# Performance work log

Measured on AMD Instinct MI355X. Metric: run time of the kernel, lower is better.

Reference implementation:

```python
import jax, jax.numpy as jnp
import numpy as np

D_MODEL = 2048
N_HEADS = 16
D_HEAD = D_MODEL // N_HEADS
B, S = 4, 2048


def setup_inputs() -> dict:
    key = jax.random.key(0)
    ks = jax.random.split(key, 5)
    scale = 1.0 / np.sqrt(D_MODEL)
    return {
        "x": jax.random.normal(ks[0], (B, S, D_MODEL), dtype=jnp.float32),
        "w_qkv": jax.random.normal(ks[1], (D_MODEL, 3 * D_MODEL), dtype=jnp.float32) * scale,
        "b_qkv": jax.random.normal(ks[2], (3 * D_MODEL,), dtype=jnp.float32) * 0.01,
        "w_out": jax.random.normal(ks[3], (D_MODEL, D_MODEL), dtype=jnp.float32) * scale,
        "b_out": jax.random.normal(ks[4], (D_MODEL,), dtype=jnp.float32) * 0.01,
    }


def reference(x, w_qkv, b_qkv, w_out, b_out):
    b, s, d = x.shape
    qkv = x @ w_qkv + b_qkv                      # [b, s, 3d]
    q, k, v = jnp.split(qkv, 3, axis=-1)
    # [b, h, s, dh]
    q = q.reshape(b, s, N_HEADS, D_HEAD).transpose(0, 2, 1, 3)
    k = k.reshape(b, s, N_HEADS, D_HEAD).transpose(0, 2, 1, 3)
    v = v.reshape(b, s, N_HEADS, D_HEAD).transpose(0, 2, 1, 3)
    # past_kv is None -> s_past == s
    scale = 1.0 / np.sqrt(D_HEAD).astype(np.float32)
    scores = jnp.einsum("bhqd,bhkd->bhqk", q, k) * scale  # [b, h, s, s]
    # causal mask: disallow j > i (diagonal = 1 + s_past - s = 1)
    causal = jnp.tril(jnp.ones((s, s), dtype=bool))
    scores = jnp.where(causal, scores, jnp.float32(-jnp.inf))
    attn = jax.nn.softmax(scores, axis=-1)
    out = jnp.einsum("bhqk,bhkd->bhqd", attn, v)          # [b, h, s, dh]
    out = out.transpose(0, 2, 1, 3).reshape(b, s, d)
    out = out @ w_out + b_out
    return out, k, v
```

## Files before the change

### kernel.cpp

```cpp
#include <hip/hip_runtime.h>
#include <hip/hip_bf16.h>
#include <cstdint>

typedef unsigned short u16;
typedef unsigned int u32;
typedef __attribute__((ext_vector_type(4))) float f32x4;
typedef __attribute__((ext_vector_type(8))) __bf16 bf16x8;

#define DEVFN static __device__ __forceinline__

constexpr int Bb = 4, S = 2048, Dm = 2048, H = 16, DH = 128;
constexpr int M  = Bb * S;
constexpr int N3 = 3 * Dm;
constexpr int KK = 2048;
constexpr float ATTN_SCALE = 0.088388347648318447f;
constexpr float LOG2E = 1.4426950408889634f;

DEVFN u16 f2bf(float f) {
  union { float f; u32 u; } v; v.f = f;
  u32 u = v.u;
  return (u16)((u + 0x7fffu + ((u >> 16) & 1u)) >> 16);
}

DEVFN void async16(const void* g, void* l) {
  __builtin_amdgcn_global_load_lds(
      (__attribute__((address_space(1))) unsigned int*)(g),
      (__attribute__((address_space(3))) unsigned int*)(l), 16, 0, 0);
}


__global__ __launch_bounds__(256) void k_cvt_bf16(const float* __restrict__ in,
                                                  u16* __restrict__ out, int n) {
  int i = (blockIdx.x * 256 + threadIdx.x) * 4;
  if (i < n) {
    float4 f = *(const float4*)(in + i);
    ushort4 o;
    o.x = f2bf(f.x); o.y = f2bf(f.y); o.z = f2bf(f.z); o.w = f2bf(f.w);
    *(ushort4*)(out + i) = o;
  }
}

__global__ __launch_bounds__(256) void k_transpose_bf16(const float* __restrict__ in,
                                                        u16* __restrict__ out,
                                                        int R, int C) {
  __shared__ float tile[32][33];
  int c0 = blockIdx.x * 32, r0 = blockIdx.y * 32;
  int tx = threadIdx.x & 31, ty = threadIdx.x >> 5;
#pragma unroll
  for (int i = 0; i < 4; i++)
    tile[ty + 8 * i][tx] = in[(size_t)(r0 + ty + 8 * i) * C + c0 + tx];
  __syncthreads();
#pragma unroll
  for (int i = 0; i < 4; i++)
    out[(size_t)(c0 + ty + 8 * i) * R + r0 + tx] = f2bf(tile[tx][ty + 8 * i]);
}


#define RA(buf, half) ((buf) * 65536 + (half) * 16384)
#define RB(buf, half) ((buf) * 65536 + 32768 + (half) * 16384)

#define BARRIER() __builtin_amdgcn_s_barrier()
#define LGK0() { asm volatile("s_waitcnt lgkmcnt(0)" ::: "memory"); __builtin_amdgcn_sched_barrier(0); }
#define VMC2() { asm volatile("s_waitcnt vmcnt(2)" ::: "memory"); __builtin_amdgcn_sched_barrier(0); }
#define VMC0() { asm volatile("s_waitcnt vmcnt(0)" ::: "memory"); __builtin_amdgcn_sched_barrier(0); }

template <int BUF, int QUAD>
DEVFN void ldAq(const char* lds, int wm, int lrow, int lkg, bf16x8 af[4][2]) {
  const char* base = lds + RA(BUF, 0) + wm * 16384;
  const int sw = (lrow & 7) << 4;
#pragma unroll
  for (int mi = 0; mi < 4; mi++) {
    int row = QUAD * 64 + mi * 16 + lrow;
#pragma unroll
    for (int kk = 0; kk < 2; kk++)
      af[mi][kk] = *(const bf16x8*)(base + row * 128 + ((kk * 64 + lkg * 16) ^ sw));
  }
}

template <int BUF, int NS>
DEVFN void ldB(const char* lds, int wn, int lrow, int lkg, bf16x8 b[2][2]) {
  const char* base = lds + RB(BUF, 0) + (wn >> 1) * 16384;
  const int sw = (lrow & 7) << 4;
#pragma unroll
  for (int ni = 0; ni < 2; ni++) {
    int row = (wn & 1) * 64 + NS * 32 + ni * 16 + lrow;
#pragma unroll
    for (int kk = 0; kk < 2; kk++)
      b[ni][kk] = *(const bf16x8*)(base + row * 128 + ((kk * 64 + lkg * 16) ^ sw));
  }
}

template <int MS, int NS>
DEVFN void mmq(f32x4 acc[8][4], bf16x8 af[4][2], bf16x8 b[2][2]) {
  __builtin_amdgcn_s_setprio(1);
#pragma unroll
  for (int kk = 0; kk < 2; kk++)
#pragma unroll
    for (int mi = 0; mi < 4; mi++)
#pragma unroll
      for (int ni = 0; ni < 2; ni++)
        acc[MS * 4 + mi][NS * 2 + ni] = __builtin_amdgcn_mfma_f32_16x16x32_bf16(
            af[mi][kk], b[ni][kk], acc[MS * 4 + mi][NS * 2 + ni], 0, 0, 0);
  __builtin_amdgcn_s_setprio(0);
}

template <int MODE>
__global__ __launch_bounds__(512, 2) void k_gemm(
    const u16* __restrict__ A, const u16* __restrict__ BT,
    const float* __restrict__ bias, float* __restrict__ Cf,
    u16* __restrict__ q_bf, u16* __restrict__ k_bf, u16* __restrict__ v_bfT,
    int N) {
  __shared__ __align__(16) char lds[131072];
  char* ldsc = lds;
  const int tid = threadIdx.x;
  const int wid = tid >> 6, lane = tid & 63;
  const int wm = wid >> 2, wn = wid & 3;
  const int lrow = lane & 15, lkg = lane >> 4;

  const int bid = blockIdx.x;
  const int xcd = bid & 7;
  const int i = bid >> 3;
  const int r = i & 15;
  const int j = i >> 4;
  const int tm0 = (xcd * 4 + (r >> 2)) << 8;
  const int tn0 = (j * 4 + (r & 3)) << 8;

  const int NT = KK >> 6;

  const int srow = tid >> 3;
  const int scol = (((tid & 7) * 16) ^ ((srow & 7) << 4)) >> 1;
  const int dstoff = (tid & ~63) * 16;
  const u16* bA0 = A + (size_t)(tm0 + srow) * KK + scol;
  const u16* bA1 = A + (size_t)(tm0 + 128 + srow) * KK + scol;
  const u16* bB0 = BT + (size_t)(tn0 + srow) * KK + scol;
  const u16* bB1 = BT + (size_t)(tn0 + 128 + srow) * KK + scol;

  auto stage2 = [&](const u16* src, int region) {
    async16(src, ldsc + region + dstoff);
    async16(src + (size_t)64 * KK, ldsc + region + 8192 + dstoff);
  };

  f32x4 acc[8][4] = {};
  bf16x8 afA[4][2], afB[4][2], b0[2][2], b1[2][2];

  stage2(bA0, RA(0, 0));
  stage2(bA1, RA(0, 1));
  stage2(bB0, RB(0, 0));
  stage2(bB1, RB(0, 1));
  stage2(bA0 + 64, RA(1, 0));
  VMC2();
  BARRIER();

  for (int it = 0; it < NT / 2; it++) {
    const int t = 2 * it;
    const int t1 = (t + 1) * 64;
    const int t2 = (t + 2 < NT) ? (t + 2) * 64 : 0;
    const int t3 = (t + 3 < NT) ? (t + 3) * 64 : 0;

    ldAq<0, 0>(ldsc, wm, lrow, lkg, afA);
    ldB<0, 0>(ldsc, wn, lrow, lkg, b0);
    stage2(bA1 + t1, RA(1, 1));
    BARRIER(); LGK0();
    mmq<0, 0>(acc, afA, b0);
    BARRIER();

    ldB<0, 1>(ldsc, wn, lrow, lkg, b1);
    stage2(bB0 + t1, RB(1, 0));
    BARRIER(); LGK0();
    mmq<0, 1>(acc, afA, b1);
    BARRIER();

    ldAq<0, 1>(ldsc, wm, lrow, lkg, afB);
    stage2(bB1 + t1, RB(1, 1));
    BARRIER(); LGK0();
    mmq<1, 1>(acc, afB, b1);
    BARRIER();

    stage2(bA0 + t2, RA(0, 0));
    VMC2();
    BARRIER();
    mmq<1, 0>(acc, afB, b0);
    BARRIER();

    ldAq<1, 0>(ldsc, wm, lrow, lkg, afA);
    ldB<1, 0>(ldsc, wn, lrow, lkg, b0);
    stage2(bA1 + t2, RA(0, 1));
    BARRIER(); LGK0();
    mmq<0, 0>(acc, afA, b0);
    BARRIER();

    ldB<1, 1>(ldsc, wn, lrow, lkg, b1);
    stage2(bB0 + t2, RB(0, 0));
    BARRIER(); LGK0();
    mmq<0, 1>(acc, afA, b1);
    BARRIER();

    ldAq<1, 1>(ldsc, wm, lrow, lkg, afB);
    stage2(bB1 + t2, RB(0, 1));
    BARRIER(); LGK0();
    mmq<1, 1>(acc, afB, b1);
    BARRIER();

    stage2(bA0 + t3, RA(1, 0));
    VMC2();
    BARRIER();
    mmq<1, 0>(acc, afB, b0);
    BARRIER();
  }
  VMC0();

  if (MODE == 0) {
#pragma unroll
    for (int mig = 0; mig < 8; mig++) {
      int row = tm0 + wm * 128 + (mig >> 2) * 64 + (mig & 3) * 16 + lkg * 4;
#pragma unroll
      for (int nig = 0; nig < 4; nig++) {
        int col = tn0 + wn * 64 + (nig >> 1) * 32 + (nig & 1) * 16 + lrow;
        float bv = bias[col];
#pragma unroll
        for (int r2 = 0; r2 < 4; r2++)
          Cf[(size_t)(row + r2) * N + col] = acc[mig][nig][r2] + bv;
      }
    }
  } else {
#pragma unroll
    for (int mig = 0; mig < 8; mig++) {
      int row = tm0 + wm * 128 + (mig >> 2) * 64 + (mig & 3) * 16 + lkg * 4;
#pragma unroll
      for (int nig = 0; nig < 4; nig++) {
        int n = tn0 + wn * 64 + (nig >> 1) * 32 + (nig & 1) * 16 + lrow;
        float bv = bias[n];
        int type = n >> 11;
        int d = n & 2047;
        int h = d >> 7, dh = d & 127;
#pragma unroll
        for (int r2 = 0; r2 < 4; r2++) {
          int rr = row + r2;
          int b = rr >> 11, s = rr & 2047;
          float val = acc[mig][nig][r2] + bv;
          size_t idx = ((size_t)(b * H + h) * S + s) * DH + dh;
          if (type == 0) {
            q_bf[idx] = f2bf(val * ATTN_SCALE);
          } else if (type == 1) {
            Cf[(size_t)M * Dm + idx] = val;
            k_bf[idx] = f2bf(val);
          } else {
            Cf[(size_t)2 * M * Dm + idx] = val;
            v_bfT[((size_t)(b * H + h) * DH + dh) * S + s] = f2bf(val);
          }
        }
      }
    }
  }
}

__global__ __launch_bounds__(256, 2) void k_attn(const u16* __restrict__ q_bf,
                                                 const u16* __restrict__ k_bf,
                                                 const u16* __restrict__ v_bfT,
                                                 u16* __restrict__ attn_bf) {
  __shared__ u16 ldsK[2][64 * 128];
  __shared__ u16 ldsV[2][128 * 64];
  __shared__ u16 ldsP[4][32 * 64];

  const int tid = threadIdx.x;
  const int wid = tid >> 6, lane = tid & 63;
  const int lrow = lane & 15, lkg = lane >> 4;

  const int bid = blockIdx.x;
  const int xcd = bid & 7;
  const int ii = bid >> 3;
  const int bh = xcd * 8 + (ii >> 4);
  const int qi = 15 - (ii & 15);
  const int b = bh >> 4, h = bh & 15;
  const int wq0 = qi * 128 + wid * 32;
  const int swz = (lrow & 7) << 4;

  const u16* qp = q_bf + (size_t)bh * S * DH;
  const u16* kp = k_bf + (size_t)bh * S * DH;
  const u16* vp = v_bfT + (size_t)bh * DH * S;

  bf16x8 qf[2][4];
#pragma unroll
  for (int qt = 0; qt < 2; qt++)
#pragma unroll
    for (int kk = 0; kk < 4; kk++)
      qf[qt][kk] = *(const bf16x8*)(qp + (size_t)(wq0 + qt * 16 + lrow) * DH +
                                    kk * 32 + lkg * 8);

  float mr[2][4], lr[2][4];
#pragma unroll
  for (int qt = 0; qt < 2; qt++)
#pragma unroll
    for (int r = 0; r < 4; r++) { mr[qt][r] = -1e30f; lr[qt][r] = 0.f; }
  f32x4 oacc[2][8] = {};

  const int nkb = qi * 2 + 2;

  auto stage = [&](int kb, int buf) {
#pragma unroll
    for (int i = 0; i < 4; i++) {
      int L = i * 4096 + wid * 1024 + lane * 16;
      int krow = L >> 8, kch = (L >> 4) & 15;
      async16(kp + (size_t)(kb * 64 + krow) * DH + ((kch ^ (krow & 7)) * 8),
              (char*)ldsK[buf] + L);
      int vd = L >> 7, vch = (L >> 4) & 7;
      async16(vp + (size_t)vd * S + kb * 64 + ((vch ^ (vd & 7)) * 8),
              (char*)ldsV[buf] + L);
    }
  };

  stage(0, 0);
  asm volatile("s_waitcnt vmcnt(0)" ::: "memory");
  __builtin_amdgcn_s_barrier();

  int cur = 0;
  for (int kb = 0; kb < nkb; kb++) {
    if (kb + 1 < nkb) stage(kb + 1, cur ^ 1);

    if (kb * 64 <= wq0 + 31) {
      const u16* Kc = ldsK[cur];
      const u16* Vc = ldsV[cur];
      f32x4 sacc[2][4] = {};
      __builtin_amdgcn_s_setprio(1);
#pragma unroll
      for (int kt = 0; kt < 4; kt++)
#pragma unroll
        for (int kk = 0; kk < 4; kk++) {
          bf16x8 kf = *(const bf16x8*)((const char*)Kc +
                        (kt * 16 + lrow) * 256 + ((kk * 64 + lkg * 16) ^ swz));
          sacc[0][kt] = __builtin_amdgcn_mfma_f32_16x16x32_bf16(qf[0][kk], kf,
                                                                sacc[0][kt], 0, 0, 0);
          sacc[1][kt] = __builtin_amdgcn_mfma_f32_16x16x32_bf16(qf[1][kk], kf,
                                                                sacc[1][kt], 0, 0, 0);
        }
      __builtin_amdgcn_s_setprio(0);

      if (kb * 64 + 63 > wq0) {
#pragma unroll
        for (int qt = 0; qt < 2; qt++)
#pragma unroll
          for (int kt = 0; kt < 4; kt++) {
            int k = kb * 64 + kt * 16 + lrow;
#pragma unroll
            for (int r = 0; r < 4; r++)
              if (k > wq0 + qt * 16 + lkg * 4 + r) sacc[qt][kt][r] = -1e30f;
          }
      }

      float pm[2][4];
#pragma unroll
      for (int qt = 0; qt < 2; qt++)
#pragma unroll
        for (int r = 0; r < 4; r++)
          pm[qt][r] = fmaxf(fmaxf(sacc[qt][0][r], sacc[qt][1][r]),
                            fmaxf(sacc[qt][2][r], sacc[qt][3][r]));
#pragma unroll
      for (int off = 1; off < 16; off <<= 1)
#pragma unroll
        for (int qt = 0; qt < 2; qt++)
#pragma unroll
          for (int r = 0; r < 4; r++)
            pm[qt][r] = fmaxf(pm[qt][r], __shfl_xor(pm[qt][r], off, 64));

      float dmax = pm[0][0] - mr[0][0];
#pragma unroll
      for (int qt = 0; qt < 2; qt++)
#pragma unroll
        for (int r = 0; r < 4; r++)
          dmax = fmaxf(dmax, pm[qt][r] - mr[qt][r]);
      if (!__all(dmax <= 8.0f)) {
        float sc[2][4];
#pragma unroll
        for (int qt = 0; qt < 2; qt++)
#pragma unroll
          for (int r = 0; r < 4; r++) {
            float mn = fmaxf(mr[qt][r], pm[qt][r]);
            sc[qt][r] = exp2f((mr[qt][r] - mn) * LOG2E);
            mr[qt][r] = mn;
            lr[qt][r] *= sc[qt][r];
          }
#pragma unroll
        for (int qt = 0; qt < 2; qt++)
#pragma unroll
          for (int nd = 0; nd < 8; nd++)
#pragma unroll
            for (int r = 0; r < 4; r++) oacc[qt][nd][r] *= sc[qt][r];
      }

      float rs[2][4] = {};
#pragma unroll
      for (int qt = 0; qt < 2; qt++)
#pragma unroll
        for (int kt = 0; kt < 4; kt++)
#pragma unroll
          for (int r = 0; r < 4; r++) {
            float p = exp2f((sacc[qt][kt][r] - mr[qt][r]) * LOG2E);
            rs[qt][r] += p;
            int prow = qt * 16 + lkg * 4 + r;
            *(u16*)((char*)ldsP[wid] + prow * 128 +
                    (((kt * 16 + lrow) * 2) ^ ((prow & 7) << 4))) = f2bf(p);
          }
#pragma unroll
      for (int off = 1; off < 16; off <<= 1)
#pragma unroll
        for (int qt = 0; qt < 2; qt++)
#pragma unroll
          for (int r = 0; r < 4; r++)
            rs[qt][r] += __shfl_xor(rs[qt][r], off, 64);
#pragma unroll
      for (int qt = 0; qt < 2; qt++)
#pragma unroll
        for (int r = 0; r < 4; r++)
          lr[qt][r] += rs[qt][r];

      asm volatile("s_waitcnt lgkmcnt(0)" ::: "memory");
      bf16x8 pf[2][2];
#pragma unroll
      for (int qt = 0; qt < 2; qt++)
#pragma unroll
        for (int kk = 0; kk < 2; kk++)
          pf[qt][kk] = *(const bf16x8*)((const char*)ldsP[wid] +
                         (qt * 16 + lrow) * 128 + ((kk * 64 + lkg * 16) ^ swz));
      __builtin_amdgcn_s_setprio(1);
#pragma unroll
      for (int nd = 0; nd < 8; nd++) {
        bf16x8 vf0 = *(const bf16x8*)((const char*)Vc +
                       (nd * 16 + lrow) * 128 + ((lkg * 16) ^ swz));
        bf16x8 vf1 = *(const bf16x8*)((const char*)Vc +
                       (nd * 16 + lrow) * 128 + ((64 + lkg * 16) ^ swz));
#pragma unroll
        for (int qt = 0; qt < 2; qt++) {
          oacc[qt][nd] = __builtin_amdgcn_mfma_f32_16x16x32_bf16(pf[qt][0], vf0,
                                                                 oacc[qt][nd], 0, 0, 0);
          oacc[qt][nd] = __builtin_amdgcn_mfma_f32_16x16x32_bf16(pf[qt][1], vf1,
                                                                 oacc[qt][nd], 0, 0, 0);
        }
      }
      __builtin_amdgcn_s_setprio(0);
    }

    asm volatile("s_waitcnt vmcnt(0)" ::: "memory");
    __builtin_amdgcn_s_barrier();
    cur ^= 1;
  }

#pragma unroll
  for (int qt = 0; qt < 2; qt++) {
    float inv[4];
#pragma unroll
    for (int r = 0; r < 4; r++) inv[r] = 1.0f / lr[qt][r];
#pragma unroll
    for (int nd = 0; nd < 8; nd++)
#pragma unroll
      for (int r = 0; r < 4; r++) {
        int q = wq0 + qt * 16 + lkg * 4 + r;
        size_t idx = ((size_t)(b * S + q) * H + h) * DH + nd * 16 + lrow;
        attn_bf[idx] = f2bf(oacc[qt][nd][r] * inv[r]);
      }
  }
}


extern "C" void kernel_launch(void* const* d_in, const int* in_sizes, int n_in,
                              void* d_out, int out_size, void* d_ws, size_t ws_size,
                              hipStream_t stream) {
  const float* x     = (const float*)d_in[0];
  const float* w_qkv = (const float*)d_in[1];
  const float* b_qkv = (const float*)d_in[2];
  const float* w_out = (const float*)d_in[3];
  const float* b_out = (const float*)d_in[4];
  float* out = (float*)d_out;

  char* ws = (char*)d_ws;
  u16* x_bf    = (u16*)ws; ws += (size_t)M * Dm * 2;
  u16* wqkvT   = (u16*)ws; ws += (size_t)N3 * Dm * 2;
  u16* woutT   = (u16*)ws; ws += (size_t)Dm * Dm * 2;
  u16* q_bf    = (u16*)ws; ws += (size_t)M * Dm * 2;
  u16* k_bf    = (u16*)ws; ws += (size_t)M * Dm * 2;
  u16* v_bfT   = (u16*)ws; ws += (size_t)M * Dm * 2;
  u16* attn_bf = (u16*)ws; ws += (size_t)M * Dm * 2;

  k_cvt_bf16<<<(M * Dm) / 1024, 256, 0, stream>>>(x, x_bf, M * Dm);
  k_transpose_bf16<<<dim3(N3 / 32, Dm / 32), 256, 0, stream>>>(w_qkv, wqkvT, Dm, N3);
  k_transpose_bf16<<<dim3(Dm / 32, Dm / 32), 256, 0, stream>>>(w_out, woutT, Dm, Dm);

  k_gemm<1><<<(N3 / 256) * (M / 256), 512, 0, stream>>>(
      x_bf, wqkvT, b_qkv, out, q_bf, k_bf, v_bfT, N3);

  k_attn<<<S / 128 * Bb * H, 256, 0, stream>>>(q_bf, k_bf, v_bfT, attn_bf);

  k_gemm<0><<<(Dm / 256) * (M / 256), 512, 0, stream>>>(
      attn_bf, woutT, b_out, out, nullptr, nullptr, nullptr, Dm);
}
```

Baseline: 552.0 us.

## Merge prep kernels, vectorize transpose stores, deepen GEMM prefetch

The x conversion and both weight transposes now run in a single launch, which removes two kernel launches and lets the three jobs share the GPU. The transpose write-back now stores four bf16 values per thread instead of one scalar each. In the GEMM main loop the async LDS stages are reordered so the B tiles load one stage earlier, and the wait threshold changes from vmcnt(2) to vmcnt(4) to keep more global loads in flight. The reordering depends on every buffer still being ready before it is read, and the new transpose store reads LDS columns that may hit bank conflicts.

```diff
diff --git a/kernel.cpp b/kernel.cpp
--- a/kernel.cpp
+++ b/kernel.cpp
@@ -29,30 +29,44 @@
 }
 
 
-__global__ __launch_bounds__(256) void k_cvt_bf16(const float* __restrict__ in,
-                                                  u16* __restrict__ out, int n) {
-  int i = (blockIdx.x * 256 + threadIdx.x) * 4;
-  if (i < n) {
-    float4 f = *(const float4*)(in + i);
-    ushort4 o;
-    o.x = f2bf(f.x); o.y = f2bf(f.y); o.z = f2bf(f.z); o.w = f2bf(f.w);
-    *(ushort4*)(out + i) = o;
-  }
-}
-
-__global__ __launch_bounds__(256) void k_transpose_bf16(const float* __restrict__ in,
-                                                        u16* __restrict__ out,
-                                                        int R, int C) {
+DEVFN void transpose_tile(const float* __restrict__ in, u16* __restrict__ out,
+                          int R, int C, int bx, int by, int tid) {
   __shared__ float tile[32][33];
-  int c0 = blockIdx.x * 32, r0 = blockIdx.y * 32;
-  int tx = threadIdx.x & 31, ty = threadIdx.x >> 5;
+  int c0 = bx * 32, r0 = by * 32;
+  int tx = tid & 31, ty = tid >> 5;
 #pragma unroll
   for (int i = 0; i < 4; i++)
     tile[ty + 8 * i][tx] = in[(size_t)(r0 + ty + 8 * i) * C + c0 + tx];
   __syncthreads();
-#pragma unroll
-  for (int i = 0; i < 4; i++)
-    out[(size_t)(c0 + ty + 8 * i) * R + r0 + tx] = f2bf(tile[tx][ty + 8 * i]);
+  int tx2 = (tid & 7) * 4, ty2 = tid >> 3;
+  ushort4 o;
+  o.x = f2bf(tile[tx2 + 0][ty2]);
+  o.y = f2bf(tile[tx2 + 1][ty2]);
+  o.z = f2bf(tile[tx2 + 2][ty2]);
+  o.w = f2bf(tile[tx2 + 3][ty2]);
+  *(ushort4*)(&out[(size_t)(c0 + ty2) * R + r0 + tx2]) = o;
+}
+
+__global__ __launch_bounds__(256) void k_prep(
+    const float* __restrict__ x, const float* __restrict__ w_qkv,
+    const float* __restrict__ w_out, u16* __restrict__ x_bf,
+    u16* __restrict__ wqkvT, u16* __restrict__ woutT) {
+  const int bid = blockIdx.x, tid = threadIdx.x;
+  constexpr int NB_CVT = (M * Dm) / 1024;
+  constexpr int NB_T1 = (N3 / 32) * (Dm / 32);
+  if (bid < NB_CVT) {
+    int i = (bid * 256 + tid) * 4;
+    float4 f = *(const float4*)(x + i);
+    ushort4 o;
+    o.x = f2bf(f.x); o.y = f2bf(f.y); o.z = f2bf(f.z); o.w = f2bf(f.w);
+    *(ushort4*)(x_bf + i) = o;
+  } else if (bid < NB_CVT + NB_T1) {
+    int b2 = bid - NB_CVT;
+    transpose_tile(w_qkv, wqkvT, Dm, N3, b2 % (N3 / 32), b2 / (N3 / 32), tid);
+  } else {
+    int b3 = bid - NB_CVT - NB_T1;
+    transpose_tile(w_out, woutT, Dm, Dm, b3 % (Dm / 32), b3 / (Dm / 32), tid);
+  }
 }
 
 
@@ -61,7 +75,7 @@
 
 #define BARRIER() __builtin_amdgcn_s_barrier()
 #define LGK0() { asm volatile("s_waitcnt lgkmcnt(0)" ::: "memory"); __builtin_amdgcn_sched_barrier(0); }
-#define VMC2() { asm volatile("s_waitcnt vmcnt(2)" ::: "memory"); __builtin_amdgcn_sched_barrier(0); }
+#define VMC4() { asm volatile("s_waitcnt vmcnt(4)" ::: "memory"); __builtin_amdgcn_sched_barrier(0); }
 #define VMC0() { asm volatile("s_waitcnt vmcnt(0)" ::: "memory"); __builtin_amdgcn_sched_barrier(0); }
 
 template <int BUF, int QUAD>
@@ -147,8 +161,9 @@
   stage2(bA1, RA(0, 1));
   stage2(bB0, RB(0, 0));
   stage2(bB1, RB(0, 1));
+  stage2(bB0 + 64, RB(1, 0));
   stage2(bA0 + 64, RA(1, 0));
-  VMC2();
+  VMC4();
   BARRIER();
 
   for (int it = 0; it < NT / 2; it++) {
@@ -159,50 +174,50 @@
 
     ldAq<0, 0>(ldsc, wm, lrow, lkg, afA);
     ldB<0, 0>(ldsc, wn, lrow, lkg, b0);
+    stage2(bB1 + t1, RB(1, 1));
+    BARRIER(); LGK0();
+    mmq<0, 0>(acc, afA, b0);
+    BARRIER();
+
+    ldB<0, 1>(ldsc, wn, lrow, lkg, b1);
     stage2(bA1 + t1, RA(1, 1));
     BARRIER(); LGK0();
+    mmq<0, 1>(acc, afA, b1);
+    BARRIER();
+
+    ldAq<0, 1>(ldsc, wm, lrow, lkg, afB);
+    stage2(bB0 + t2, RB(0, 0));
+    BARRIER(); LGK0();
+    mmq<1, 1>(acc, afB, b1);
+    BARRIER();
+
+    stage2(bB1 + t2, RB(0, 1));
+    VMC4();
+    BARRIER();
+    mmq<1, 0>(acc, afB, b0);
+    BARRIER();
+
+    ldAq<1, 0>(ldsc, wm, lrow, lkg, afA);
+    ldB<1, 0>(ldsc, wn, lrow, lkg, b0);
+    stage2(bA0 + t2, RA(0, 0));
+    BARRIER(); LGK0();
     mmq<0, 0>(acc, afA, b0);
     BARRIER();
 
-    ldB<0, 1>(ldsc, wn, lrow, lkg, b1);
-    stage2(bB0 + t1, RB(1, 0));
+    ldB<1, 1>(ldsc, wn, lrow, lkg, b1);
+    stage2(bA1 + t2, RA(0, 1));
     BARRIER(); LGK0();
     mmq<0, 1>(acc, afA, b1);
     BARRIER();
 
-    ldAq<0, 1>(ldsc, wm, lrow, lkg, afB);
-    stage2(bB1 + t1, RB(1, 1));
+    ldAq<1, 1>(ldsc, wm, lrow, lkg, afB);
+    stage2(bB0 + t3, RB(1, 0));
     BARRIER(); LGK0();
     mmq<1, 1>(acc, afB, b1);
     BARRIER();
 
-    stage2(bA0 + t2, RA(0, 0));
-    VMC2();
-    BARRIER();
-    mmq<1, 0>(acc, afB, b0);
-    BARRIER();
-
-    ldAq<1, 0>(ldsc, wm, lrow, lkg, afA);
-    ldB<1, 0>(ldsc, wn, lrow, lkg, b0);
-    stage2(bA1 + t2, RA(0, 1));
-    BARRIER(); LGK0();
-    mmq<0, 0>(acc, afA, b0);
-    BARRIER();
-
-    ldB<1, 1>(ldsc, wn, lrow, lkg, b1);
-    stage2(bB0 + t2, RB(0, 0));
-    BARRIER(); LGK0();
-    mmq<0, 1>(acc, afA, b1);
-    BARRIER();
-
-    ldAq<1, 1>(ldsc, wm, lrow, lkg, afB);
-    stage2(bB1 + t2, RB(0, 1));
-    BARRIER(); LGK0();
-    mmq<1, 1>(acc, afB, b1);
-    BARRIER();
-
     stage2(bA0 + t3, RA(1, 0));
-    VMC2();
+    VMC4();
     BARRIER();
     mmq<1, 0>(acc, afB, b0);
     BARRIER();
@@ -480,9 +495,9 @@
   u16* v_bfT   = (u16*)ws; ws += (size_t)M * Dm * 2;
   u16* attn_bf = (u16*)ws; ws += (size_t)M * Dm * 2;
 
-  k_cvt_bf16<<<(M * Dm) / 1024, 256, 0, stream>>>(x, x_bf, M * Dm);
-  k_transpose_bf16<<<dim3(N3 / 32, Dm / 32), 256, 0, stream>>>(w_qkv, wqkvT, Dm, N3);
-  k_transpose_bf16<<<dim3(Dm / 32, Dm / 32), 256, 0, stream>>>(w_out, woutT, Dm, Dm);
+  constexpr int NB_PREP = (M * Dm) / 1024 + (N3 / 32) * (Dm / 32) +
+                          (Dm / 32) * (Dm / 32);
+  k_prep<<<NB_PREP, 256, 0, stream>>>(x, w_qkv, w_out, x_bf, wqkvT, woutT);
 
   k_gemm<1><<<(N3 / 256) * (M / 256), 512, 0, stream>>>(
       x_bf, wqkvT, b_qkv, out, q_bf, k_bf, v_bfT, N3);
```

After: 545.1 us. No clear change (-1.3%).
